# Kernel tuning notes

Measured on AMD Instinct MI355X. Metric: run time of the kernel, lower is better.

The kernel has to match this reference:

```python
import jax, jax.numpy as jnp
import numpy as np

N_NODES, IN_F, HIDDEN, N_EDGES, N_TRAIN, N_CLASS = 50000, 64, 512, 160000, 80000, 7
BN_EPS = 1e-5

def _lin(k, fin, fout):
    return jax.random.normal(k, (fin, fout), jnp.float32) * 0.05, jnp.zeros((fout,), jnp.float32)

def setup_inputs() -> dict:
    key = jax.random.key(0)
    ks = jax.random.split(key, 12)
    x = jax.random.normal(ks[0], (N_NODES, IN_F), jnp.float32)
    edge_index = jax.random.randint(ks[1], (2, N_EDGES), 0, N_NODES, jnp.int32)
    train_edge_id = jax.random.randint(ks[2], (N_TRAIN,), 0, N_EDGES, jnp.int32)
    W1, b1 = _lin(ks[3], IN_F, HIDDEN)
    W2, b2 = _lin(ks[4], HIDDEN, HIDDEN)
    W3, b3 = _lin(ks[5], HIDDEN, HIDDEN)
    W4, b4 = _lin(ks[6], HIDDEN, HIDDEN)
    lin1_W, lin1_b = _lin(ks[7], HIDDEN, HIDDEN)
    lin2_W, lin2_b = _lin(ks[8], HIDDEN, HIDDEN)
    fc2_W, fc2_b = _lin(ks[9], HIDDEN, N_CLASS)
    ones = jnp.ones((HIDDEN,), jnp.float32); zeros = jnp.zeros((HIDDEN,), jnp.float32)
    return dict(x=x, edge_index=edge_index, train_edge_id=train_edge_id,
                W1=W1, b1=b1, W2=W2, b2=b2, W3=W3, b3=b3,
                bn1_g=ones, bn1_b=zeros, bn1_m=zeros, bn1_v=ones, eps1=jnp.float32(0.0),
                W4=W4, b4=b4, bn2_g=ones, bn2_b=zeros, bn2_m=zeros, bn2_v=ones, eps2=jnp.float32(0.0),
                lin1_W=lin1_W, lin1_b=lin1_b, lin2_W=lin2_W, lin2_b=lin2_b,
                fc2_W=fc2_W, fc2_b=fc2_b)

def _gin_agg(h, src, dst, eps):
    # PyG GINConv: (1+eps)*x_i + sum_{j in N(i)} x_j, messages flow src->dst
    agg = jax.ops.segment_sum(h[src], dst, num_segments=N_NODES)
    return (1.0 + eps) * h + agg

def _bn(h, g, b, m, v):
    return (h - m) * jax.lax.rsqrt(v + BN_EPS) * g + b

def reference(x, edge_index, train_edge_id, W1, b1, W2, b2, W3, b3,
              bn1_g, bn1_b, bn1_m, bn1_v, eps1,
              W4, b4, bn2_g, bn2_b, bn2_m, bn2_v, eps2,
              lin1_W, lin1_b, lin2_W, lin2_b, fc2_W, fc2_b):
    src, dst = edge_index[0], edge_index[1]
    h = _gin_agg(x, src, dst, eps1)
    h = jax.nn.relu(h @ W1 + b1)
    h = jax.nn.relu(h @ W2 + b2)
    h = jax.nn.relu(h @ W3 + b3)
    h = _bn(h, bn1_g, bn1_b, bn1_m, bn1_v)
    # gin_convs[0]: agg -> Linear+ReLU -> BN
    h = _gin_agg(h, src, dst, eps2)
    h = jax.nn.relu(h @ W4 + b4)
    h = _bn(h, bn2_g, bn2_b, bn2_m, bn2_v)
    # node MLP head (dropout = identity in eval)
    h = jax.nn.relu(h @ lin1_W + lin1_b)
    h = h @ lin2_W + lin2_b
    # edge-gather fusion (feature_fusion=None -> elementwise mul)
    node_id = edge_index[:, train_edge_id]  # [2, T]
    x1 = h[node_id[0]]
    x2 = h[node_id[1]]
    return (x1 * x2) @ fc2_W + fc2_b  # [T, class_num]
```

## Files before the change

### kernel.cpp

```cpp
#include <hip/hip_runtime.h>

#define N_NODES 50000
#define MPAD    50048
#define IN_F    64
#define HIDDEN  512
#define N_EDGES 160000
#define N_TRAIN 80000
#define N_CLASS 7
#define BN_EPS  1e-5f

#define MT      (MPAD / 128)
#define NT      4
#define FULLGRP ((MT / 8) * 32)
#define NBLK    ((N_NODES + 255) / 256)

#define MT2     ((MPAD + 255) / 256)
#define FULLG2  ((MT2 / 8) * 32)
#define NG2     (MT2 * 4)

typedef short  bf16x8 __attribute__((ext_vector_type(8)));
typedef float  f32x4  __attribute__((ext_vector_type(4)));
typedef unsigned short ushort_t;

__device__ __forceinline__ ushort_t f2b(float v) {
    union { float f; unsigned int u; } c; c.f = v;
    unsigned int x = c.u;
    unsigned int r = (x + 0x7FFFu + ((x >> 16) & 1u)) >> 16;
    return (ushort_t)r;
}
__device__ __forceinline__ float b2f(ushort_t b) {
    union { unsigned int u; float f; } c; c.u = ((unsigned int)b) << 16;
    return c.f;
}

__device__ __forceinline__ void async_copy16(const void* g, void* l) {
    __builtin_amdgcn_global_load_lds(
        (const __attribute__((address_space(1))) void*)g,
        (__attribute__((address_space(3))) void*)l, 16, 0, 0);
}

__global__ void zero_kernel(int* __restrict__ p, int n) {
    int i = blockIdx.x * blockDim.x + threadIdx.x;
    if (i < n) p[i] = 0;
}

__global__ void hist_kernel(const int* __restrict__ ei, int* __restrict__ deg) {
    int e = blockIdx.x * blockDim.x + threadIdx.x;
    if (e >= N_EDGES) return;
    atomicAdd(&deg[ei[N_EDGES + e]], 1);
}

__global__ __launch_bounds__(256) void blocksum_kernel(const int* __restrict__ deg,
                                                       int* __restrict__ bsum) {
    __shared__ int s[256];
    int i = blockIdx.x * 256 + threadIdx.x;
    s[threadIdx.x] = (i < N_NODES) ? deg[i] : 0;
    __syncthreads();
    for (int off = 128; off > 0; off >>= 1) {
        if (threadIdx.x < off) s[threadIdx.x] += s[threadIdx.x + off];
        __syncthreads();
    }
    if (threadIdx.x == 0) bsum[blockIdx.x] = s[0];
}

__global__ __launch_bounds__(256) void scanbsum_kernel(const int* __restrict__ bsum,
                                                       int* __restrict__ boff) {
    __shared__ int s[256];
    int tid = threadIdx.x;
    s[tid] = (tid < NBLK) ? bsum[tid] : 0;
    __syncthreads();
    for (int off = 1; off < 256; off <<= 1) {
        int t = (tid >= off) ? s[tid - off] : 0;
        __syncthreads();
        s[tid] += t;
        __syncthreads();
    }
    if (tid < NBLK) boff[tid] = (tid == 0) ? 0 : s[tid - 1];
}

__global__ __launch_bounds__(256) void rowptr_kernel(const int* __restrict__ deg,
                                                     const int* __restrict__ boff,
                                                     int* __restrict__ rowptr,
                                                     int* __restrict__ cursor) {
    __shared__ int s[256];
    int tid = threadIdx.x;
    int i = blockIdx.x * 256 + tid;
    int d = (i < N_NODES) ? deg[i] : 0;
    s[tid] = d;
    __syncthreads();
    for (int off = 1; off < 256; off <<= 1) {
        int t = (tid >= off) ? s[tid - off] : 0;
        __syncthreads();
        s[tid] += t;
        __syncthreads();
    }
    int incl = s[tid] + boff[blockIdx.x];
    if (i < N_NODES) {
        rowptr[i + 1] = incl;
        cursor[i] = incl - d;
    }
    if (i == 0) rowptr[0] = 0;
}

__global__ void scatter_kernel(const int* __restrict__ ei,
                               int* __restrict__ cursor, int* __restrict__ adj) {
    int e = blockIdx.x * blockDim.x + threadIdx.x;
    if (e >= N_EDGES) return;
    int src = ei[e], dst = ei[N_EDGES + e];
    int pos = atomicAdd(&cursor[dst], 1);
    adj[pos] = src;
}

__global__ __launch_bounds__(256) void gather64_kernel(
    const float* __restrict__ x, const int* __restrict__ rowptr,
    const int* __restrict__ adj, const float* __restrict__ epsp,
    ushort_t* __restrict__ hi, ushort_t* __restrict__ lo) {
    int wave = threadIdx.x >> 6, lane = threadIdx.x & 63;
    int n = blockIdx.x * 4 + wave;
    if (n >= N_NODES) return;
    float s = 1.0f + *epsp;
    float sum = s * x[(size_t)n * IN_F + lane];
    int beg = rowptr[n], end = rowptr[n + 1];
    for (int k = beg; k < end; k++) {
        sum += x[(size_t)adj[k] * IN_F + lane];
    }
    ushort_t hb = f2b(sum);
    ushort_t lb = f2b(sum - b2f(hb));
    hi[(size_t)n * IN_F + lane] = hb;
    lo[(size_t)n * IN_F + lane] = lb;
}

__global__ __launch_bounds__(256) void gather512_kernel(
    const float* __restrict__ h, const int* __restrict__ rowptr,
    const int* __restrict__ adj, const float* __restrict__ epsp,
    ushort_t* __restrict__ hi, ushort_t* __restrict__ lo) {
    int wave = threadIdx.x >> 6, lane = threadIdx.x & 63;
    int n = blockIdx.x * 2 + (wave >> 1);
    if (n >= N_NODES) return;
    float s = 1.0f + *epsp;
    const int f = (wave & 1) * 256 + lane * 4;
    float4 a = *(const float4*)&h[(size_t)n * HIDDEN + f];
    float sum[4] = {s * a.x, s * a.y, s * a.z, s * a.w};
    int beg = rowptr[n], end = rowptr[n + 1];
    for (int k = beg; k < end; k++) {
        float4 b = *(const float4*)&h[(size_t)adj[k] * HIDDEN + f];
        sum[0] += b.x; sum[1] += b.y; sum[2] += b.z; sum[3] += b.w;
    }
    ushort_t h4[4], l4[4];
#pragma unroll
    for (int j = 0; j < 4; j++) {
        h4[j] = f2b(sum[j]);
        l4[j] = f2b(sum[j] - b2f(h4[j]));
    }
    *(ushort4*)&hi[(size_t)n * HIDDEN + f] = make_ushort4(h4[0], h4[1], h4[2], h4[3]);
    *(ushort4*)&lo[(size_t)n * HIDDEN + f] = make_ushort4(l4[0], l4[1], l4[2], l4[3]);
}

__global__ void wtrans_all_kernel(const float* __restrict__ w0,
                                  const float* __restrict__ w1,
                                  const float* __restrict__ w2,
                                  const float* __restrict__ w3,
                                  const float* __restrict__ w4,
                                  const float* __restrict__ w5,
                                  ushort_t* __restrict__ Wp) {
    const size_t WSMALL = (size_t)HIDDEN * IN_F;
    const size_t WBIG   = (size_t)HIDDEN * HIDDEN;
    int z = blockIdx.z;
    const float* W = (z == 0) ? w0 : (z == 1) ? w1 : (z == 2) ? w2
                   : (z == 3) ? w3 : (z == 4) ? w4 : w5;
    int K = (z == 0) ? IN_F : HIDDEN;
    size_t off_h = (z == 0) ? 0 : 2 * WSMALL + (size_t)(z - 1) * 2 * WBIG;
    ushort_t* Whi = Wp + off_h;
    ushort_t* Wlo = Whi + ((z == 0) ? WSMALL : WBIG);

    __shared__ float t[32][33];
    int tx = threadIdx.x & 31, ty = threadIdx.x >> 5;
    int nb = blockIdx.x * 32, kb = blockIdx.y * 32;
    if (kb >= K) return;
#pragma unroll
    for (int i = 0; i < 4; i++) {
        int k = kb + ty + i * 8;
        t[ty + i * 8][tx] = W[(size_t)k * HIDDEN + nb + tx];
    }
    __syncthreads();
#pragma unroll
    for (int i = 0; i < 4; i++) {
        int n = nb + ty + i * 8;
        int k = kb + tx;
        float v = t[tx][ty + i * 8];
        ushort_t hb = f2b(v);
        ushort_t lb = f2b(v - b2f(hb));
        Whi[(size_t)n * K + k] = hb;
        Wlo[(size_t)n * K + k] = lb;
    }
}

__global__ __launch_bounds__(512, 2) void gemm_split8_kernel(
    const ushort_t* __restrict__ Ahi, const ushort_t* __restrict__ Alo,
    const ushort_t* __restrict__ Bhi, const ushort_t* __restrict__ Blo,
    const float* __restrict__ bias,
    float* __restrict__ Cf, ushort_t* __restrict__ Chi, ushort_t* __restrict__ Clo,
    int mode,
    const float* __restrict__ bn_g, const float* __restrict__ bn_b,
    const float* __restrict__ bn_m, const float* __restrict__ bn_v) {
    const int K = HIDDEN;
    __shared__ ushort_t As_h[3][256 * 32];
    __shared__ ushort_t As_l[3][256 * 32];
    __shared__ ushort_t Bs_h[3][128 * 32];
    __shared__ ushort_t Bs_l[3][128 * 32];

    const int tid  = threadIdx.x;
    const int wave = tid >> 6, lane = tid & 63;
    const int wm = wave >> 1, wn = wave & 1;
    const int quad = lane >> 4, r = lane & 15;

    int idx = blockIdx.x, m_t, n_t;
    if (idx < FULLG2) {
        m_t = (idx >> 5) * 8 + (idx & 7);
        n_t = (idx >> 3) & 3;
    } else {
        int t2 = idx - FULLG2;
        m_t = (FULLG2 >> 2) + (t2 >> 2);
        n_t = t2 & 3;
    }
    const int m0 = m_t * 256, n0 = n_t * 128;

    const f32x4 vzero = {0.f, 0.f, 0.f, 0.f};
    f32x4 acc[4][4];
#pragma unroll
    for (int i = 0; i < 4; i++)
#pragma unroll
        for (int j = 0; j < 4; j++) acc[i][j] = vzero;

    const int srow = lane >> 2;
    const int scol = (((lane & 3) + ((srow >> 1) & 3)) & 3) * 8;
    const int csw  = ((quad - ((r >> 1) & 3)) & 3) * 8;

    auto stage = [&](int kt, int b) {
        const int k0 = kt * 32;
#pragma unroll
        for (int tt = 0; tt < 2; tt++) {
            int rra = wave * 32 + tt * 16 + srow;
            int lba = (wave * 32 + tt * 16) * 32;
            size_t ga = (size_t)(m0 + rra) * K + k0 + scol;
            async_copy16(Ahi + ga, &As_h[b][lba]);
            async_copy16(Alo + ga, &As_l[b][lba]);
        }
        {
            int rrb = wave * 16 + srow;
            int lbb = (wave * 16) * 32;
            size_t gb = (size_t)(n0 + rrb) * K + k0 + scol;
            async_copy16(Bhi + gb, &Bs_h[b][lbb]);
            async_copy16(Blo + gb, &Bs_l[b][lbb]);
        }
    };

    stage(0, 0);
    stage(1, 1);
    asm volatile("s_waitcnt vmcnt(6)" ::: "memory");
    __builtin_amdgcn_s_barrier();

#pragma unroll
    for (int t = 0; t < 16; t++) {
        const int cur = t % 3;
        if (t + 2 < 16) stage(t + 2, (t + 2) % 3);

        bf16x8 ah[4], bh[4], al[4], bl[4];
#pragma unroll
        for (int i = 0; i < 4; i++) {
            int aofs = (wm * 64 + i * 16 + r) * 32 + csw;
            ah[i] = *(const bf16x8*)&As_h[cur][aofs];
        }
#pragma unroll
        for (int j = 0; j < 4; j++) {
            int bofs = (wn * 64 + j * 16 + r) * 32 + csw;
            bh[j] = *(const bf16x8*)&Bs_h[cur][bofs];
        }
        __builtin_amdgcn_s_setprio(1);
#pragma unroll
        for (int i = 0; i < 4; i++)
#pragma unroll
            for (int j = 0; j < 4; j++)
                acc[i][j] = __builtin_amdgcn_mfma_f32_16x16x32_bf16(ah[i], bh[j], acc[i][j], 0, 0, 0);
        __builtin_amdgcn_s_setprio(0);
#pragma unroll
        for (int j = 0; j < 4; j++) {
            int bofs = (wn * 64 + j * 16 + r) * 32 + csw;
            bl[j] = *(const bf16x8*)&Bs_l[cur][bofs];
        }
        __builtin_amdgcn_s_setprio(1);
#pragma unroll
        for (int i = 0; i < 4; i++)
#pragma unroll
            for (int j = 0; j < 4; j++)
                acc[i][j] = __builtin_amdgcn_mfma_f32_16x16x32_bf16(ah[i], bl[j], acc[i][j], 0, 0, 0);
        __builtin_amdgcn_s_setprio(0);
#pragma unroll
        for (int i = 0; i < 4; i++) {
            int aofs = (wm * 64 + i * 16 + r) * 32 + csw;
            al[i] = *(const bf16x8*)&As_l[cur][aofs];
        }
        __builtin_amdgcn_s_setprio(1);
#pragma unroll
        for (int i = 0; i < 4; i++)
#pragma unroll
            for (int j = 0; j < 4; j++)
                acc[i][j] = __builtin_amdgcn_mfma_f32_16x16x32_bf16(al[i], bh[j], acc[i][j], 0, 0, 0);
        __builtin_amdgcn_s_setprio(0);

        if (t < 15) {
            if (t < 14) asm volatile("s_waitcnt vmcnt(6)" ::: "memory");
            else        asm volatile("s_waitcnt vmcnt(0)" ::: "memory");
            __builtin_amdgcn_s_barrier();
        }
    }

    float bia[4], sc[4], sh[4];
#pragma unroll
    for (int j = 0; j < 4; j++) {
        int col = n0 + wn * 64 + j * 16 + r;
        bia[j] = bias[col];
        if (mode == 2) {
            float g = bn_g[col], bb = bn_b[col], mm = bn_m[col], vv = bn_v[col];
            sc[j] = g * rsqrtf(vv + BN_EPS);
            sh[j] = bb - mm * sc[j];
        } else { sc[j] = 1.f; sh[j] = 0.f; }
    }
#pragma unroll
    for (int i = 0; i < 4; i++) {
#pragma unroll
        for (int rg = 0; rg < 4; rg++) {
            int row = m0 + wm * 64 + i * 16 + quad * 4 + rg;
            if (row >= N_NODES) continue;
#pragma unroll
            for (int j = 0; j < 4; j++) {
                int col = n0 + wn * 64 + j * 16 + r;
                float v = acc[i][j][rg] + bia[j];
                if (mode >= 1) v = fmaxf(v, 0.f);
                if (mode == 2) v = v * sc[j] + sh[j];
                size_t oix = (size_t)row * HIDDEN + col;
                if (Cf) {
                    Cf[oix] = v;
                } else {
                    ushort_t hb = f2b(v);
                    ushort_t lb = f2b(v - b2f(hb));
                    Chi[oix] = hb;
                    Clo[oix] = lb;
                }
            }
        }
    }
}

__global__ __launch_bounds__(256) void gemm_k64_kernel(
    const ushort_t* __restrict__ Ahi, const ushort_t* __restrict__ Alo,
    const ushort_t* __restrict__ Bhi, const ushort_t* __restrict__ Blo,
    const float* __restrict__ bias,
    ushort_t* __restrict__ Chi, ushort_t* __restrict__ Clo) {
    const int K = 64;
    __shared__ ushort_t As_h[128 * 64];
    __shared__ ushort_t As_l[128 * 64];
    __shared__ ushort_t Bs_h[128 * 64];
    __shared__ ushort_t Bs_l[128 * 64];

    const int tid  = threadIdx.x;
    const int wave = tid >> 6, lane = tid & 63;
    const int wm = wave >> 1, wn = wave & 1;
    const int quad = lane >> 4, r = lane & 15;

    int idx = blockIdx.x, m_t, n_t;
    if (idx < FULLGRP) {
        m_t = (idx >> 5) * 8 + (idx & 7);
        n_t = (idx >> 3) & 3;
    } else {
        int t = idx - FULLGRP;
        m_t = (FULLGRP >> 2) + (t >> 2);
        n_t = t & 3;
    }
    const int m0 = m_t * 128, n0 = n_t * 128;

    const int srow8 = lane >> 3;
    const int sc8   = (((lane & 7) - srow8) & 7) * 8;
#pragma unroll
    for (int t = 0; t < 4; t++) {
        int base = wave * 32 + t * 8;
        int rr = base + srow8;
        int lbase = base * 64;
        size_t ga = (size_t)(m0 + rr) * K + sc8;
        size_t gb = (size_t)(n0 + rr) * K + sc8;
        async_copy16(Ahi + ga, &As_h[lbase]);
        async_copy16(Alo + ga, &As_l[lbase]);
        async_copy16(Bhi + gb, &Bs_h[lbase]);
        async_copy16(Blo + gb, &Bs_l[lbase]);
    }
    __syncthreads();

    const f32x4 vzero = {0.f, 0.f, 0.f, 0.f};
    f32x4 acc[4][4];
#pragma unroll
    for (int i = 0; i < 4; i++)
#pragma unroll
        for (int j = 0; j < 4; j++) acc[i][j] = vzero;

#pragma unroll
    for (int ks = 0; ks < 2; ks++) {
        bf16x8 ah[4], al[4], bh[4], bl[4];
#pragma unroll
        for (int i = 0; i < 4; i++) {
            int ra = wm * 64 + i * 16 + r;
            int rb = wn * 64 + i * 16 + r;
            int ca = ((quad + ks * 4 + (ra & 7)) & 7) * 8;
            int cb = ((quad + ks * 4 + (rb & 7)) & 7) * 8;
            ah[i] = *(const bf16x8*)&As_h[ra * 64 + ca];
            al[i] = *(const bf16x8*)&As_l[ra * 64 + ca];
            bh[i] = *(const bf16x8*)&Bs_h[rb * 64 + cb];
            bl[i] = *(const bf16x8*)&Bs_l[rb * 64 + cb];
        }
#pragma unroll
        for (int i = 0; i < 4; i++)
#pragma unroll
            for (int j = 0; j < 4; j++) {
                acc[i][j] = __builtin_amdgcn_mfma_f32_16x16x32_bf16(ah[i], bh[j], acc[i][j], 0, 0, 0);
                acc[i][j] = __builtin_amdgcn_mfma_f32_16x16x32_bf16(ah[i], bl[j], acc[i][j], 0, 0, 0);
                acc[i][j] = __builtin_amdgcn_mfma_f32_16x16x32_bf16(al[i], bh[j], acc[i][j], 0, 0, 0);
            }
    }

    float bia[4];
#pragma unroll
    for (int j = 0; j < 4; j++) bia[j] = bias[n0 + wn * 64 + j * 16 + r];
#pragma unroll
    for (int i = 0; i < 4; i++) {
#pragma unroll
        for (int rg = 0; rg < 4; rg++) {
            int row = m0 + wm * 64 + i * 16 + quad * 4 + rg;
            if (row >= N_NODES) continue;
#pragma unroll
            for (int j = 0; j < 4; j++) {
                int col = n0 + wn * 64 + j * 16 + r;
                float v = fmaxf(acc[i][j][rg] + bia[j], 0.f);
                size_t oix = (size_t)row * HIDDEN + col;
                ushort_t hb = f2b(v);
                ushort_t lb = f2b(v - b2f(hb));
                Chi[oix] = hb;
                Clo[oix] = lb;
            }
        }
    }
}

__global__ __launch_bounds__(256) void fc2_kernel(
    const float* __restrict__ h, const int* __restrict__ ei,
    const int* __restrict__ teid, const float* __restrict__ W,
    const float* __restrict__ bias, float* __restrict__ out) {
    __shared__ float Ws[HIDDEN * N_CLASS];
    __shared__ float bs[N_CLASS];
    for (int i = threadIdx.x; i < HIDDEN * N_CLASS; i += blockDim.x) Ws[i] = W[i];
    if (threadIdx.x < N_CLASS) bs[threadIdx.x] = bias[threadIdx.x];
    __syncthreads();

    int wave = threadIdx.x >> 6;
    int lane = threadIdx.x & 63;
    int t = blockIdx.x * 4 + wave;
    if (t >= N_TRAIN) return;

    int e = teid[t];
    int a = ei[e];
    int b = ei[N_EDGES + e];
    const float* xa = h + (size_t)a * HIDDEN;
    const float* xb = h + (size_t)b * HIDDEN;

    float acc[N_CLASS];
#pragma unroll
    for (int c = 0; c < N_CLASS; c++) acc[c] = 0.f;

    int j0 = lane * 8;
    float4 a0 = *(const float4*)&xa[j0];
    float4 a1 = *(const float4*)&xa[j0 + 4];
    float4 b0 = *(const float4*)&xb[j0];
    float4 b1 = *(const float4*)&xb[j0 + 4];
    float p[8] = {a0.x * b0.x, a0.y * b0.y, a0.z * b0.z, a0.w * b0.w,
                  a1.x * b1.x, a1.y * b1.y, a1.z * b1.z, a1.w * b1.w};
#pragma unroll
    for (int jj = 0; jj < 8; jj++) {
        const float* wrow = &Ws[(j0 + jj) * N_CLASS];
#pragma unroll
        for (int c = 0; c < N_CLASS; c++) acc[c] = fmaf(p[jj], wrow[c], acc[c]);
    }
#pragma unroll
    for (int c = 0; c < N_CLASS; c++) {
        float v = acc[c];
        for (int off = 32; off > 0; off >>= 1) v += __shfl_down(v, off, 64);
        if (lane == 0) out[(size_t)t * N_CLASS + c] = v + bs[c];
    }
}

extern "C" void kernel_launch(void* const* d_in, const int* in_sizes, int n_in,
                              void* d_out, int out_size, void* d_ws, size_t ws_size,
                              hipStream_t stream) {
    const float* x      = (const float*)d_in[0];
    const int*   ei     = (const int*)d_in[1];
    const int*   teid   = (const int*)d_in[2];
    const float* W1     = (const float*)d_in[3];
    const float* b1     = (const float*)d_in[4];
    const float* W2     = (const float*)d_in[5];
    const float* b2     = (const float*)d_in[6];
    const float* W3     = (const float*)d_in[7];
    const float* b3     = (const float*)d_in[8];
    const float* bn1_g  = (const float*)d_in[9];
    const float* bn1_b  = (const float*)d_in[10];
    const float* bn1_m  = (const float*)d_in[11];
    const float* bn1_v  = (const float*)d_in[12];
    const float* eps1   = (const float*)d_in[13];
    const float* W4     = (const float*)d_in[14];
    const float* b4     = (const float*)d_in[15];
    const float* bn2_g  = (const float*)d_in[16];
    const float* bn2_b  = (const float*)d_in[17];
    const float* bn2_m  = (const float*)d_in[18];
    const float* bn2_v  = (const float*)d_in[19];
    const float* eps2   = (const float*)d_in[20];
    const float* lin1_W = (const float*)d_in[21];
    const float* lin1_b = (const float*)d_in[22];
    const float* lin2_W = (const float*)d_in[23];
    const float* lin2_b = (const float*)d_in[24];
    const float* fc2_W  = (const float*)d_in[25];
    const float* fc2_b  = (const float*)d_in[26];

    const size_t PLANE   = (size_t)MPAD * HIDDEN;
    const size_t PLANE64 = (size_t)MPAD * IN_F;

    ushort_t* R0h = (ushort_t*)d_ws;
    ushort_t* R0l = R0h + PLANE;
    ushort_t* R1h = R0l + PLANE;
    ushort_t* R1l = R1h + PLANE;

    const size_t WSMALL = (size_t)HIDDEN * IN_F;
    const size_t WBIG   = (size_t)HIDDEN * HIDDEN;
    ushort_t* Wp   = R1l + PLANE;
    ushort_t* Wt1h = Wp;            ushort_t* Wt1l = Wt1h + WSMALL;
    ushort_t* Wt2h = Wt1l + WSMALL; ushort_t* Wt2l = Wt2h + WBIG;
    ushort_t* Wt3h = Wt2l + WBIG;   ushort_t* Wt3l = Wt3h + WBIG;
    ushort_t* Wt4h = Wt3l + WBIG;   ushort_t* Wt4l = Wt4h + WBIG;
    ushort_t* Wt5h = Wt4l + WBIG;   ushort_t* Wt5l = Wt5h + WBIG;
    ushort_t* Wt6h = Wt5l + WBIG;   ushort_t* Wt6l = Wt6h + WBIG;

    int* deg    = (int*)(Wt6l + WBIG);
    int* cursor = deg + N_NODES;
    int* rowptr = cursor + N_NODES;
    int* bsum   = rowptr + (N_NODES + 1);
    int* boff   = bsum + NBLK;
    int* adj    = boff + NBLK;

    float* F32_R0 = (float*)R0h;
    ushort_t* H0h = R1h;
    ushort_t* H0l = R1h + PLANE64;

    zero_kernel<<<(N_NODES + 255) / 256, 256, 0, stream>>>(deg, N_NODES);
    hist_kernel<<<(N_EDGES + 255) / 256, 256, 0, stream>>>(ei, deg);
    blocksum_kernel<<<NBLK, 256, 0, stream>>>(deg, bsum);
    scanbsum_kernel<<<1, 256, 0, stream>>>(bsum, boff);
    rowptr_kernel<<<NBLK, 256, 0, stream>>>(deg, boff, rowptr, cursor);
    scatter_kernel<<<(N_EDGES + 255) / 256, 256, 0, stream>>>(ei, cursor, adj);

    wtrans_all_kernel<<<dim3(16, 16, 6), 256, 0, stream>>>(W1, W2, W3, W4,
                                                           lin1_W, lin2_W, Wp);

    const int ngrid = MT * NT;
    int nwb = (N_NODES + 3) / 4;

    gather64_kernel<<<nwb, 256, 0, stream>>>(x, rowptr, adj, eps1, H0h, H0l);

    gemm_k64_kernel<<<ngrid, 256, 0, stream>>>(H0h, H0l, Wt1h, Wt1l, b1, R0h, R0l);
    gemm_split8_kernel<<<NG2, 512, 0, stream>>>(R0h, R0l, Wt2h, Wt2l, b2,
        nullptr, R1h, R1l, 1, nullptr, nullptr, nullptr, nullptr);
    gemm_split8_kernel<<<NG2, 512, 0, stream>>>(R1h, R1l, Wt3h, Wt3l, b3,
        F32_R0, nullptr, nullptr, 2, bn1_g, bn1_b, bn1_m, bn1_v);

    gather512_kernel<<<(N_NODES + 1) / 2, 256, 0, stream>>>(F32_R0, rowptr, adj,
                                                            eps2, R1h, R1l);

    gemm_split8_kernel<<<NG2, 512, 0, stream>>>(R1h, R1l, Wt4h, Wt4l, b4,
        nullptr, R0h, R0l, 2, bn2_g, bn2_b, bn2_m, bn2_v);
    gemm_split8_kernel<<<NG2, 512, 0, stream>>>(R0h, R0l, Wt5h, Wt5l, lin1_b,
        nullptr, R1h, R1l, 1, nullptr, nullptr, nullptr, nullptr);
    gemm_split8_kernel<<<NG2, 512, 0, stream>>>(R1h, R1l, Wt6h, Wt6l, lin2_b,
        F32_R0, nullptr, nullptr, 0, nullptr, nullptr, nullptr, nullptr);

    fc2_kernel<<<(N_TRAIN + 3) / 4, 256, 0, stream>>>(F32_R0, ei, teid, fc2_W, fc2_b,
                                                      (float*)d_out);
}
```

Measured before the change: 968.5 us.

## Interleave async prefetch chunks with MFMA phases using ping-pong barriers

Splits the per-iteration global-to-LDS prefetch into three chunks (two A halves and B) and issues each between the LDS reads and the MFMA block of one of the three compute phases. Scheduling barriers and extra workgroup barriers are added around each MFMA phase, so waves alternate between memory issue and math in a ping-pong style. The aim is to spread memory issue across the iteration and overlap it better with matrix work. The cost is several extra s_barrier calls per k-step, which could add stalls.

```diff
diff --git a/kernel.cpp b/kernel.cpp
--- a/kernel.cpp
+++ b/kernel.cpp
@@ -236,36 +236,36 @@
     const int scol = (((lane & 3) + ((srow >> 1) & 3)) & 3) * 8;
     const int csw  = ((quad - ((r >> 1) & 3)) & 3) * 8;
 
-    auto stage = [&](int kt, int b) {
+    auto stageA = [&](int kt, int b, int tt) {
         const int k0 = kt * 32;
-#pragma unroll
-        for (int tt = 0; tt < 2; tt++) {
-            int rra = wave * 32 + tt * 16 + srow;
-            int lba = (wave * 32 + tt * 16) * 32;
-            size_t ga = (size_t)(m0 + rra) * K + k0 + scol;
-            async_copy16(Ahi + ga, &As_h[b][lba]);
-            async_copy16(Alo + ga, &As_l[b][lba]);
-        }
-        {
-            int rrb = wave * 16 + srow;
-            int lbb = (wave * 16) * 32;
-            size_t gb = (size_t)(n0 + rrb) * K + k0 + scol;
-            async_copy16(Bhi + gb, &Bs_h[b][lbb]);
-            async_copy16(Blo + gb, &Bs_l[b][lbb]);
-        }
+        int rra = wave * 32 + tt * 16 + srow;
+        int lba = (wave * 32 + tt * 16) * 32;
+        size_t ga = (size_t)(m0 + rra) * K + k0 + scol;
+        async_copy16(Ahi + ga, &As_h[b][lba]);
+        async_copy16(Alo + ga, &As_l[b][lba]);
     };
-
-    stage(0, 0);
-    stage(1, 1);
+    auto stageB = [&](int kt, int b) {
+        const int k0 = kt * 32;
+        int rrb = wave * 16 + srow;
+        int lbb = (wave * 16) * 32;
+        size_t gb = (size_t)(n0 + rrb) * K + k0 + scol;
+        async_copy16(Bhi + gb, &Bs_h[b][lbb]);
+        async_copy16(Blo + gb, &Bs_l[b][lbb]);
+    };
+
+    stageA(0, 0, 0); stageA(0, 0, 1); stageB(0, 0);
+    stageA(1, 1, 0); stageA(1, 1, 1); stageB(1, 1);
     asm volatile("s_waitcnt vmcnt(6)" ::: "memory");
     __builtin_amdgcn_s_barrier();
 
 #pragma unroll
     for (int t = 0; t < 16; t++) {
         const int cur = t % 3;
-        if (t + 2 < 16) stage(t + 2, (t + 2) % 3);
+        const int nb2 = (t + 2) % 3;
+        const bool pf = (t + 2 < 16);
 
         bf16x8 ah[4], bh[4], al[4], bl[4];
+
 #pragma unroll
         for (int i = 0; i < 4; i++) {
             int aofs = (wm * 64 + i * 16 + r) * 32 + csw;
@@ -276,6 +276,9 @@
             int bofs = (wn * 64 + j * 16 + r) * 32 + csw;
             bh[j] = *(const bf16x8*)&Bs_h[cur][bofs];
         }
+        if (pf) stageA(t + 2, nb2, 0);
+        __builtin_amdgcn_sched_barrier(0);
+        __builtin_amdgcn_s_barrier();
         __builtin_amdgcn_s_setprio(1);
 #pragma unroll
         for (int i = 0; i < 4; i++)
@@ -283,11 +286,17 @@
             for (int j = 0; j < 4; j++)
                 acc[i][j] = __builtin_amdgcn_mfma_f32_16x16x32_bf16(ah[i], bh[j], acc[i][j], 0, 0, 0);
         __builtin_amdgcn_s_setprio(0);
+        __builtin_amdgcn_s_barrier();
+        __builtin_amdgcn_sched_barrier(0);
+
 #pragma unroll
         for (int j = 0; j < 4; j++) {
             int bofs = (wn * 64 + j * 16 + r) * 32 + csw;
             bl[j] = *(const bf16x8*)&Bs_l[cur][bofs];
         }
+        if (pf) stageA(t + 2, nb2, 1);
+        __builtin_amdgcn_sched_barrier(0);
+        __builtin_amdgcn_s_barrier();
         __builtin_amdgcn_s_setprio(1);
 #pragma unroll
         for (int i = 0; i < 4; i++)
@@ -295,11 +304,17 @@
             for (int j = 0; j < 4; j++)
                 acc[i][j] = __builtin_amdgcn_mfma_f32_16x16x32_bf16(ah[i], bl[j], acc[i][j], 0, 0, 0);
         __builtin_amdgcn_s_setprio(0);
+        __builtin_amdgcn_s_barrier();
+        __builtin_amdgcn_sched_barrier(0);
+
 #pragma unroll
         for (int i = 0; i < 4; i++) {
             int aofs = (wm * 64 + i * 16 + r) * 32 + csw;
             al[i] = *(const bf16x8*)&As_l[cur][aofs];
         }
+        if (pf) stageB(t + 2, nb2);
+        __builtin_amdgcn_sched_barrier(0);
+        __builtin_amdgcn_s_barrier();
         __builtin_amdgcn_s_setprio(1);
 #pragma unroll
         for (int i = 0; i < 4; i++)
@@ -312,6 +327,7 @@
             if (t < 14) asm volatile("s_waitcnt vmcnt(6)" ::: "memory");
             else        asm volatile("s_waitcnt vmcnt(0)" ::: "memory");
             __builtin_amdgcn_s_barrier();
+            __builtin_amdgcn_sched_barrier(0);
         }
     }
 
```

After: 961.3 us. About the same (-0.7%).
